# Kernel tuning notes

Measured on AMD Instinct MI355X. Metric: run time of the kernel, lower is better.

## Reference

```python
import jax, jax.numpy as jnp
import numpy as np

N, E = 20000, 200000
HID, NH, L = 128, 8, 7
DH = HID // NH
SCALE = float(np.sqrt(DH))
NNUM = 5
MLP_IN = HID + HID + 8 + 8 + 8 + NNUM  # 285
EPS = 1e-5


def _ln(x, g, b):
    mu = jnp.mean(x, -1, keepdims=True)
    var = jnp.mean((x - mu) ** 2, -1, keepdims=True)
    return (x - mu) * jax.lax.rsqrt(var + EPS) * g + b


def setup_inputs() -> dict:
    key = jax.random.key(0)
    ks = jax.random.split(key, 24)
    f = lambda k, s: (0.05 * jax.random.normal(k, s)).astype(jnp.float32)
    z = lambda s: jnp.zeros(s, jnp.float32)
    o = lambda s: jnp.ones(s, jnp.float32)
    inp = {
        'node_feats': f(ks[0], (N, 2)),
        'numericals': f(ks[1], (E, NNUM)),
        'W_emb': f(ks[2], (2, HID)), 'b_emb': z((HID,)),
        'WQ': f(ks[3], (L, HID, HID)), 'bQ': z((L, HID)),
        'WK': f(ks[4], (L, HID, HID)), 'bK': z((L, HID)),
        'WV': f(ks[5], (L, HID, HID)), 'bV': z((L, HID)),
        'WO': f(ks[6], (L, HID, HID)), 'bO': z((L, HID)),
        'ln1_g': o((L, HID)), 'ln1_b': z((L, HID)),
        'ln2_g': o((L, HID)), 'ln2_b': z((L, HID)),
        'W1': f(ks[7], (L, HID, HID)), 'b1': z((L, HID)),
        'W2': f(ks[8], (L, HID, HID)), 'b2': z((L, HID)),
        'curr_emb': f(ks[9], (15, 8)), 'pay_emb': f(ks[10], (7, 8)),
        'mlp_Wh': f(ks[11], (3, MLP_IN, MLP_IN)), 'mlp_bh': z((3, MLP_IN)),
        'mlp_Wo': f(ks[12], (MLP_IN, 2)), 'mlp_bo': z((2,)),
        'src': jax.random.randint(ks[13], (E,), 0, N, dtype=jnp.int32),
        'dst': jax.random.randint(ks[14], (E,), 0, N, dtype=jnp.int32),
        'payment_currency': jax.random.randint(ks[15], (E,), 0, 15, dtype=jnp.int32),
        'receiving_currency': jax.random.randint(ks[16], (E,), 0, 15, dtype=jnp.int32),
        'payment_format': jax.random.randint(ks[17], (E,), 0, 7, dtype=jnp.int32),
    }
    return inp


def reference(node_feats, numericals, W_emb, b_emb, WQ, bQ, WK, bK, WV, bV, WO, bO,
              ln1_g, ln1_b, ln2_g, ln2_b, W1, b1, W2, b2, curr_emb, pay_emb,
              mlp_Wh, mlp_bh, mlp_Wo, mlp_bo, src, dst,
              payment_currency, receiving_currency, payment_format):
    h = node_feats @ W_emb + b_emb  # [N, HID]
    for l in range(L):
        # --- graph multi-head attention (segment softmax over in-edges of dst) ---
        x = _ln(h, ln1_g[l], ln1_b[l])
        Q = (x @ WQ[l] + bQ[l]).reshape(N, NH, DH)
        K = (x @ WK[l] + bK[l]).reshape(N, NH, DH)
        V = (x @ WV[l] + bV[l]).reshape(N, NH, DH)
        scores = jnp.einsum('ehd,ehd->eh', Q[dst], K[src]) / SCALE  # [E, NH]
        m = jax.ops.segment_max(scores, dst, num_segments=N)        # [N, NH]
        ex = jnp.exp(scores - m[dst])
        den = jax.ops.segment_sum(ex, dst, num_segments=N)
        w = ex / den[dst]                                           # attn weights per edge
        attn = jax.ops.segment_sum(w[:, :, None] * V[src], dst, num_segments=N)
        h = h + attn.reshape(N, HID) @ WO[l] + bO[l]
        # --- FFN ---
        x = _ln(h, ln2_g[l], ln2_b[l])
        h = h + jax.nn.relu(x @ W1[l] + b1[l]) @ W2[l] + b2[l]
    # --- edge classifier ---
    ef = jnp.concatenate([curr_emb[payment_currency], curr_emb[receiving_currency],
                          pay_emb[payment_format], numericals], axis=1)  # [E, 29]
    y = jnp.concatenate([h[src], h[dst], ef], axis=1)  # [E, 285]
    for i in range(3):
        y = jax.nn.relu(y @ mlp_Wh[i] + mlp_bh[i])
    return y @ mlp_Wo + mlp_bo  # [E, 2]
```

## Files before the change

kernel.cpp:

```cpp
#include <hip/hip_runtime.h>

#define HID 128
#define NH 8
#define DH 16
#define NLAYERS 7
#define MLP_IN 285
#define MP 288
#define LDW 296
#define XS 136

typedef short short8 __attribute__((ext_vector_type(8)));
typedef float f32x4 __attribute__((ext_vector_type(4)));
typedef float f32x16 __attribute__((ext_vector_type(16)));
typedef unsigned short ushort8 __attribute__((ext_vector_type(8)));

__device__ inline unsigned short f2bf(float f) {
    union { float f; unsigned int u; } v; v.f = f;
    unsigned int r = v.u + 0x7FFF + ((v.u >> 16) & 1);
    return (unsigned short)(r >> 16);
}
__device__ inline float bf2f(unsigned short u) {
    union { unsigned int u; float f; } v; v.u = ((unsigned int)u) << 16;
    return v.f;
}

__global__ __launch_bounds__(256) void embed_kernel(
    const float* __restrict__ nf, const float* __restrict__ We,
    const float* __restrict__ be, float* __restrict__ h, int N)
{
    int idx = blockIdx.x * 256 + threadIdx.x;
    if (idx >= N * HID) return;
    int n = idx >> 7, j = idx & 127;
    h[idx] = fmaf(nf[n * 2], We[j], fmaf(nf[n * 2 + 1], We[HID + j], be[j]));
}

__global__ __launch_bounds__(256) void prep_nodew_kernel(
    const float* __restrict__ WQ, const float* __restrict__ WK,
    const float* __restrict__ WV, const float* __restrict__ WO,
    const float* __restrict__ W1, const float* __restrict__ W2,
    unsigned short* __restrict__ wnh, unsigned short* __restrict__ wnl)
{
    int idx = blockIdx.x * 256 + threadIdx.x;
    if (idx >= 42 * 32 * 64) return;
    int lane = idx & 63;
    int r = idx >> 6;
    int kt = r & 7; r >>= 3;
    int ct = r & 3; r >>= 2;
    int m = r;
    int l = m / 6, wi = m - l * 6;
    const float* Wb;
    switch (wi) {
        case 0: Wb = WQ; break; case 1: Wb = WK; break; case 2: Wb = WV; break;
        case 3: Wb = WO; break; case 4: Wb = W1; break; default: Wb = W2; break;
    }
    Wb += (size_t)l * HID * HID;
    int n = ct * 32 + (lane & 31);
    int kb = kt * 16 + (lane >> 5) * 8;
    ushort8 vh, vl;
#pragma unroll
    for (int j = 0; j < 8; ++j) {
        float w = Wb[(size_t)(kb + j) * HID + n];
        unsigned short hi = f2bf(w);
        vh[j] = hi;
        vl[j] = f2bf(w - bf2f(hi));
    }
    *(ushort8*)&wnh[(size_t)idx * 8] = vh;
    *(ushort8*)&wnl[(size_t)idx * 8] = vl;
}

#define LOADB(m, BH, BL) do { \
    size_t fb_ = (((size_t)(matbase + (m)) * 32 + (size_t)wave * 8) * 64 + lane) * 8; \
    const unsigned short* Bh_ = wnh + fb_; \
    const unsigned short* Bl_ = wnl + fb_; \
    _Pragma("unroll") \
    for (int kt = 0; kt < 8; ++kt) { \
        BH[kt] = *(const short8*)&Bh_[kt * 512]; \
        BL[kt] = *(const short8*)&Bl_[kt * 512]; \
    } \
} while (0)

#define COMPSTORE(BH, BL, BIAS, OUT, STRIDE, OFF) do { \
    f32x16 acc = {}; \
    _Pragma("unroll") \
    for (int kt = 0; kt < 8; ++kt) \
        acc = __builtin_amdgcn_mfma_f32_32x32x16_bf16(ah[kt], BH[kt], acc, 0, 0, 0); \
    _Pragma("unroll") \
    for (int kt = 0; kt < 8; ++kt) \
        acc = __builtin_amdgcn_mfma_f32_32x32x16_bf16(al[kt], BH[kt], acc, 0, 0, 0); \
    _Pragma("unroll") \
    for (int kt = 0; kt < 8; ++kt) \
        acc = __builtin_amdgcn_mfma_f32_32x32x16_bf16(ah[kt], BL[kt], acc, 0, 0, 0); \
    int col_ = wave * 32 + l31; \
    float bv_ = (BIAS)[col_]; \
    _Pragma("unroll") \
    for (int r = 0; r < 16; ++r) { \
        int rowm_ = (r & 3) + 8 * (r >> 2) + 4 * half; \
        int row_ = rowBase + rowm_; \
        if (row_ < M) (OUT)[(size_t)row_ * (STRIDE) + (OFF) + col_] = acc[r] + bv_; \
    } \
} while (0)

__global__ __launch_bounds__(256, 2) void ln_qkv_mfma(
    const float* __restrict__ h,
    const float* __restrict__ g, const float* __restrict__ bb,
    const unsigned short* __restrict__ wnh, const unsigned short* __restrict__ wnl,
    int matbase,
    const float* __restrict__ bQ, const float* __restrict__ bK, const float* __restrict__ bV,
    float* __restrict__ qo, float* __restrict__ kvo, int M)
{
    __shared__ unsigned short Xh[32][XS];
    __shared__ unsigned short Xl[32][XS];
    int tid = threadIdx.x;
    int lane = tid & 63, wave = tid >> 6;
    int rowBase = blockIdx.x * 32;

    for (int i = 0; i < 8; ++i) {
        int r = wave * 8 + i;
        int row = rowBase + r;
        float a0 = 0.f, a1 = 0.f;
        if (row < M) {
            a0 = h[(size_t)row * HID + lane];
            a1 = h[(size_t)row * HID + 64 + lane];
        }
        float s = a0 + a1;
#pragma unroll
        for (int off = 32; off > 0; off >>= 1) s += __shfl_down(s, off, 64);
        s = __shfl(s, 0, 64);
        float mu = s * (1.0f / 128.0f);
        float d0 = a0 - mu, d1 = a1 - mu;
        float v = d0 * d0 + d1 * d1;
#pragma unroll
        for (int off = 32; off > 0; off >>= 1) v += __shfl_down(v, off, 64);
        v = __shfl(v, 0, 64);
        float rr = rsqrtf(v * (1.0f / 128.0f) + 1e-5f);
        float x0 = d0 * rr * g[lane] + bb[lane];
        float x1 = d1 * rr * g[64 + lane] + bb[64 + lane];
        unsigned short h0 = f2bf(x0), h1 = f2bf(x1);
        Xh[r][lane] = h0;           Xh[r][64 + lane] = h1;
        Xl[r][lane] = f2bf(x0 - bf2f(h0));
        Xl[r][64 + lane] = f2bf(x1 - bf2f(h1));
    }
    __syncthreads();

    int l31 = lane & 31;
    int half = lane >> 5;

    short8 ah[8], al[8];
#pragma unroll
    for (int kt = 0; kt < 8; ++kt) {
        ah[kt] = *(const short8*)&Xh[l31][kt * 16 + half * 8];
        al[kt] = *(const short8*)&Xl[l31][kt * 16 + half * 8];
    }

    short8 bh0[8], bl0[8], bh1[8], bl1[8];
    LOADB(0, bh0, bl0);
    LOADB(1, bh1, bl1);
    COMPSTORE(bh0, bl0, bQ, qo, HID, 0);
    LOADB(2, bh0, bl0);
    COMPSTORE(bh1, bl1, bK, kvo, 256, 0);
    COMPSTORE(bh0, bl0, bV, kvo, 256, 128);
}

__global__ __launch_bounds__(256, 2) void post_qkv_mfma(
    const float* __restrict__ at, const float* __restrict__ hin,
    const unsigned short* __restrict__ wnh, const unsigned short* __restrict__ wnl,
    int matbase,
    const float* __restrict__ bO,
    const float* __restrict__ g2, const float* __restrict__ b2g,
    const float* __restrict__ b1, const float* __restrict__ b2,
    float* __restrict__ hout,
    int doQkv,
    const float* __restrict__ g1n, const float* __restrict__ b1n,
    const float* __restrict__ bQn, const float* __restrict__ bKn, const float* __restrict__ bVn,
    float* __restrict__ qout, float* __restrict__ kvout,
    unsigned short* __restrict__ hbout,
    int M)
{
    __shared__ unsigned short Ah[32][XS];
    __shared__ unsigned short Al[32][XS];
    __shared__ unsigned short Th[32][XS];
    __shared__ unsigned short Tl[32][XS];
    __shared__ float Hs[32][132];
    int tid = threadIdx.x;
    int lane = tid & 63, wave = tid >> 6;
    int rowBase = blockIdx.x * 32;
    int l31 = lane & 31;
    int half = lane >> 5;

    for (int i = tid; i < 32 * 32; i += 256) {
        int r = i >> 5, c4 = i & 31;
        int row = rowBase + r;
        float4 va = make_float4(0.f, 0.f, 0.f, 0.f), vh = va;
        if (row < M) {
            va = *(const float4*)&at[(size_t)row * HID + c4 * 4];
            vh = *(const float4*)&hin[(size_t)row * HID + c4 * 4];
        }
        const float* vp = (const float*)&va;
#pragma unroll
        for (int q = 0; q < 4; ++q) {
            unsigned short hi = f2bf(vp[q]);
            Ah[r][c4 * 4 + q] = hi;
            Al[r][c4 * 4 + q] = f2bf(vp[q] - bf2f(hi));
        }
        *(float4*)&Hs[r][c4 * 4] = vh;
    }
    __syncthreads();

    int colW = wave * 32 + l31;

    {
        short8 ah[8], al[8];
#pragma unroll
        for (int kt = 0; kt < 8; ++kt) {
            ah[kt] = *(const short8*)&Ah[l31][kt * 16 + half * 8];
            al[kt] = *(const short8*)&Al[l31][kt * 16 + half * 8];
        }
        short8 bh[8], bl[8];
        {
            size_t fb = (((size_t)(matbase + 3) * 32 + (size_t)wave * 8) * 64 + lane) * 8;
            const unsigned short* Bh = wnh + fb;
            const unsigned short* Bl = wnl + fb;
#pragma unroll
            for (int kt = 0; kt < 8; ++kt) {
                bh[kt] = *(const short8*)&Bh[kt * 512];
                bl[kt] = *(const short8*)&Bl[kt * 512];
            }
        }
        f32x16 acc = {};
#pragma unroll
        for (int kt = 0; kt < 8; ++kt)
            acc = __builtin_amdgcn_mfma_f32_32x32x16_bf16(ah[kt], bh[kt], acc, 0, 0, 0);
#pragma unroll
        for (int kt = 0; kt < 8; ++kt)
            acc = __builtin_amdgcn_mfma_f32_32x32x16_bf16(al[kt], bh[kt], acc, 0, 0, 0);
#pragma unroll
        for (int kt = 0; kt < 8; ++kt)
            acc = __builtin_amdgcn_mfma_f32_32x32x16_bf16(ah[kt], bl[kt], acc, 0, 0, 0);
        float bv = bO[colW];
#pragma unroll
        for (int r = 0; r < 16; ++r) {
            int rowm = (r & 3) + 8 * (r >> 2) + 4 * half;
            Hs[rowm][colW] += acc[r] + bv;
        }
    }
    __syncthreads();

    for (int i = 0; i < 8; ++i) {
        int r = wave * 8 + i;
        float a0 = Hs[r][lane];
        float a1 = Hs[r][64 + lane];
        float s = a0 + a1;
#pragma unroll
        for (int off = 32; off > 0; off >>= 1) s += __shfl_down(s, off, 64);
        s = __shfl(s, 0, 64);
        float mu = s * (1.0f / 128.0f);
        float d0 = a0 - mu, d1 = a1 - mu;
        float v = d0 * d0 + d1 * d1;
#pragma unroll
        for (int off = 32; off > 0; off >>= 1) v += __shfl_down(v, off, 64);
        v = __shfl(v, 0, 64);
        float rr = rsqrtf(v * (1.0f / 128.0f) + 1e-5f);
        float x0 = d0 * rr * g2[lane] + b2g[lane];
        float x1 = d1 * rr * g2[64 + lane] + b2g[64 + lane];
        unsigned short h0 = f2bf(x0), h1 = f2bf(x1);
        Ah[r][lane] = h0;           Ah[r][64 + lane] = h1;
        Al[r][lane] = f2bf(x0 - bf2f(h0));
        Al[r][64 + lane] = f2bf(x1 - bf2f(h1));
    }
    __syncthreads();

    {
        short8 ah[8], al[8];
#pragma unroll
        for (int kt = 0; kt < 8; ++kt) {
            ah[kt] = *(const short8*)&Ah[l31][kt * 16 + half * 8];
            al[kt] = *(const short8*)&Al[l31][kt * 16 + half * 8];
        }
        short8 bh[8], bl[8];
        {
            size_t fb = (((size_t)(matbase + 4) * 32 + (size_t)wave * 8) * 64 + lane) * 8;
            const unsigned short* Bh = wnh + fb;
            const unsigned short* Bl = wnl + fb;
#pragma unroll
            for (int kt = 0; kt < 8; ++kt) {
                bh[kt] = *(const short8*)&Bh[kt * 512];
                bl[kt] = *(const short8*)&Bl[kt * 512];
            }
        }
        f32x16 acc = {};
#pragma unroll
        for (int kt = 0; kt < 8; ++kt)
            acc = __builtin_amdgcn_mfma_f32_32x32x16_bf16(ah[kt], bh[kt], acc, 0, 0, 0);
#pragma unroll
        for (int kt = 0; kt < 8; ++kt)
            acc = __builtin_amdgcn_mfma_f32_32x32x16_bf16(al[kt], bh[kt], acc, 0, 0, 0);
#pragma unroll
        for (int kt = 0; kt < 8; ++kt)
            acc = __builtin_amdgcn_mfma_f32_32x32x16_bf16(ah[kt], bl[kt], acc, 0, 0, 0);
        float bv = b1[colW];
#pragma unroll
        for (int r = 0; r < 16; ++r) {
            int rowm = (r & 3) + 8 * (r >> 2) + 4 * half;
            float t = fmaxf(acc[r] + bv, 0.f);
            unsigned short hi = f2bf(t);
            Th[rowm][colW] = hi;
            Tl[rowm][colW] = f2bf(t - bf2f(hi));
        }
    }
    __syncthreads();

    {
        short8 ah[8], al[8];
#pragma unroll
        for (int kt = 0; kt < 8; ++kt) {
            ah[kt] = *(const short8*)&Th[l31][kt * 16 + half * 8];
            al[kt] = *(const short8*)&Tl[l31][kt * 16 + half * 8];
        }
        short8 bh[8], bl[8];
        {
            size_t fb = (((size_t)(matbase + 5) * 32 + (size_t)wave * 8) * 64 + lane) * 8;
            const unsigned short* Bh = wnh + fb;
            const unsigned short* Bl = wnl + fb;
#pragma unroll
            for (int kt = 0; kt < 8; ++kt) {
                bh[kt] = *(const short8*)&Bh[kt * 512];
                bl[kt] = *(const short8*)&Bl[kt * 512];
            }
        }
        f32x16 acc = {};
#pragma unroll
        for (int kt = 0; kt < 8; ++kt)
            acc = __builtin_amdgcn_mfma_f32_32x32x16_bf16(ah[kt], bh[kt], acc, 0, 0, 0);
#pragma unroll
        for (int kt = 0; kt < 8; ++kt)
            acc = __builtin_amdgcn_mfma_f32_32x32x16_bf16(al[kt], bh[kt], acc, 0, 0, 0);
#pragma unroll
        for (int kt = 0; kt < 8; ++kt)
            acc = __builtin_amdgcn_mfma_f32_32x32x16_bf16(ah[kt], bl[kt], acc, 0, 0, 0);
        float bv = b2[colW];
#pragma unroll
        for (int r = 0; r < 16; ++r) {
            int rowm = (r & 3) + 8 * (r >> 2) + 4 * half;
            int row = rowBase + rowm;
            float hn = Hs[rowm][colW] + acc[r] + bv;
            Hs[rowm][colW] = hn;
            if (row < M) {
                if (doQkv) hout[(size_t)row * HID + colW] = hn;
                else       hbout[(size_t)row * HID + colW] = f2bf(hn);
            }
        }
    }

    if (!doQkv) return;
    __syncthreads();

    for (int i = 0; i < 8; ++i) {
        int r = wave * 8 + i;
        float a0 = Hs[r][lane];
        float a1 = Hs[r][64 + lane];
        float s = a0 + a1;
#pragma unroll
        for (int off = 32; off > 0; off >>= 1) s += __shfl_down(s, off, 64);
        s = __shfl(s, 0, 64);
        float mu = s * (1.0f / 128.0f);
        float d0 = a0 - mu, d1 = a1 - mu;
        float v = d0 * d0 + d1 * d1;
#pragma unroll
        for (int off = 32; off > 0; off >>= 1) v += __shfl_down(v, off, 64);
        v = __shfl(v, 0, 64);
        float rr = rsqrtf(v * (1.0f / 128.0f) + 1e-5f);
        float x0 = d0 * rr * g1n[lane] + b1n[lane];
        float x1 = d1 * rr * g1n[64 + lane] + b1n[64 + lane];
        unsigned short h0 = f2bf(x0), h1 = f2bf(x1);
        Ah[r][lane] = h0;           Ah[r][64 + lane] = h1;
        Al[r][lane] = f2bf(x0 - bf2f(h0));
        Al[r][64 + lane] = f2bf(x1 - bf2f(h1));
    }
    __syncthreads();

    {
        short8 ah[8], al[8];
#pragma unroll
        for (int kt = 0; kt < 8; ++kt) {
            ah[kt] = *(const short8*)&Ah[l31][kt * 16 + half * 8];
            al[kt] = *(const short8*)&Al[l31][kt * 16 + half * 8];
        }
        short8 bh0[8], bl0[8], bh1[8], bl1[8];
        LOADB(6, bh0, bl0);
        LOADB(7, bh1, bl1);
        COMPSTORE(bh0, bl0, bQn, qout, HID, 0);
        LOADB(8, bh0, bl0);
        COMPSTORE(bh1, bl1, bKn, kvout, 256, 0);
        COMPSTORE(bh0, bl0, bVn, kvout, 256, 128);
    }
}

__global__ __launch_bounds__(256) void deg_kernel(
    const int* __restrict__ dst, int* __restrict__ deg, int E)
{
    int e = blockIdx.x * 256 + threadIdx.x;
    if (e < E) atomicAdd(&deg[dst[e]], 1);
}

__global__ __launch_bounds__(256) void scan_kernel(
    const int* __restrict__ deg, int* __restrict__ rowptr,
    int* __restrict__ cursor, int N)
{
    __shared__ int sums[256];
    int tid = threadIdx.x;
    int chunk = (N + 255) / 256;
    int lo = tid * chunk;
    int hi = lo + chunk; if (hi > N) hi = N;
    int s = 0;
    for (int i = lo; i < hi && i >= 0; ++i) s += deg[i];
    sums[tid] = s;
    __syncthreads();
    for (int off = 1; off < 256; off <<= 1) {
        int v = (tid >= off) ? sums[tid - off] : 0;
        __syncthreads();
        sums[tid] += v;
        __syncthreads();
    }
    int base = (tid == 0) ? 0 : sums[tid - 1];
    for (int i = lo; i < hi; ++i) {
        rowptr[i] = base; cursor[i] = base; base += deg[i];
    }
    if (tid == 255) rowptr[N] = sums[255];
}

__global__ __launch_bounds__(256) void scatter_kernel(
    const int* __restrict__ src, const int* __restrict__ dst,
    int* __restrict__ cursor, int* __restrict__ ssrc, int E)
{
    int e = blockIdx.x * 256 + threadIdx.x;
    if (e < E) {
        int p = atomicAdd(&cursor[dst[e]], 1);
        ssrc[p] = src[e];
    }
}

__global__ __launch_bounds__(256) void attn_fused_kernel(
    const float* __restrict__ q, const float* __restrict__ kv,
    const int* __restrict__ rowptr, const int* __restrict__ ssrc,
    float* __restrict__ at, int N)
{
    int node = blockIdx.x * 4 + (threadIdx.x >> 6);
    int lane = threadIdx.x & 63;
    if (node >= N) return;
    int beg = rowptr[node], end = rowptr[node + 1];
    float q0 = q[(size_t)node * HID + lane];
    float q1 = q[(size_t)node * HID + 64 + lane];
    float acc0 = 0.f, acc1 = 0.f, den0 = 0.f, den1 = 0.f;
    int i = beg;
    for (; i + 2 <= end; i += 2) {
        int s0 = ssrc[i], s1 = ssrc[i + 1];
        const float* kv0 = kv + (size_t)s0 * 256;
        const float* kv1 = kv + (size_t)s1 * 256;
        float k00 = kv0[lane],       k01 = kv0[64 + lane];
        float v00 = kv0[128 + lane], v01 = kv0[192 + lane];
        float k10 = kv1[lane],       k11 = kv1[64 + lane];
        float v10 = kv1[128 + lane], v11 = kv1[192 + lane];
        float p00 = q0 * k00, p01 = q1 * k01;
        float p10 = q0 * k10, p11 = q1 * k11;
#pragma unroll
        for (int off = 1; off < 16; off <<= 1) {
            p00 += __shfl_xor(p00, off, 64);
            p01 += __shfl_xor(p01, off, 64);
            p10 += __shfl_xor(p10, off, 64);
            p11 += __shfl_xor(p11, off, 64);
        }
        float w00 = __expf(p00 * 0.25f), w01 = __expf(p01 * 0.25f);
        float w10 = __expf(p10 * 0.25f), w11 = __expf(p11 * 0.25f);
        den0 += w00 + w10; den1 += w01 + w11;
        acc0 = fmaf(w10, v10, fmaf(w00, v00, acc0));
        acc1 = fmaf(w11, v11, fmaf(w01, v01, acc1));
    }
    if (i < end) {
        int s = ssrc[i];
        const float* kv0 = kv + (size_t)s * 256;
        float k0 = kv0[lane], k1 = kv0[64 + lane];
        float p0 = q0 * k0, p1 = q1 * k1;
#pragma unroll
        for (int off = 1; off < 16; off <<= 1) {
            p0 += __shfl_xor(p0, off, 64);
            p1 += __shfl_xor(p1, off, 64);
        }
        float w0 = __expf(p0 * 0.25f), w1 = __expf(p1 * 0.25f);
        den0 += w0; den1 += w1;
        acc0 = fmaf(w0, kv0[128 + lane], acc0);
        acc1 = fmaf(w1, kv0[192 + lane], acc1);
    }
    at[(size_t)node * HID + lane]      = (den0 > 0.f) ? acc0 / den0 : 0.f;
    at[(size_t)node * HID + 64 + lane] = (den1 > 0.f) ? acc1 / den1 : 0.f;
}

__global__ __launch_bounds__(256) void prep_wp_kernel(
    const float* __restrict__ Wh, unsigned short* __restrict__ wp)
{
    int idx = blockIdx.x * 256 + threadIdx.x;
    if (idx >= 3 * 9 * 18 * 64) return;
    int lane = idx & 63;
    int r = idx >> 6;
    int kt = r % 18; r /= 18;
    int ct = r % 9;
    int layer = r / 9;
    int n = ct * 32 + (lane & 31);
    int kbase = kt * 16 + (lane >> 5) * 8;
    ushort8 val;
#pragma unroll
    for (int j = 0; j < 8; ++j) {
        int k = kbase + j;
        float v = (n < MLP_IN && k < MLP_IN)
            ? Wh[(size_t)layer * MLP_IN * MLP_IN + (size_t)k * MLP_IN + n] : 0.f;
        val[j] = f2bf(v);
    }
    *(ushort8*)&wp[(size_t)idx * 8] = val;
}

__global__ __launch_bounds__(256, 3) void edge_mlp_mfma(
    const unsigned short* __restrict__ hb, const float* __restrict__ ce,
    const float* __restrict__ pe, const float* __restrict__ num,
    const int* __restrict__ src, const int* __restrict__ dst,
    const int* __restrict__ pc, const int* __restrict__ rc,
    const int* __restrict__ pf,
    const unsigned short* __restrict__ wp, const float* __restrict__ bh,
    const float* __restrict__ Wo, const float* __restrict__ bo,
    float* __restrict__ out, int E)
{
    __shared__ unsigned short y[64 * LDW];
    __shared__ float sc[2][32][33];
    int tid = threadIdx.x;
    int e0 = blockIdx.x * 64;
    int wave = tid >> 6;
    int lane = tid & 63;
    int l31 = lane & 31;
    int half = lane >> 5;

    for (int i = tid; i < 64 * 36; i += 256) {
        int t = i / 36;
        int c = i - t * 36;
        int e = e0 + t;
        if (e >= E) e = E - 1;
        ushort8 val;
        if (c < 16) {
            val = *(const ushort8*)&hb[(size_t)src[e] * HID + c * 8];
        } else if (c < 32) {
            val = *(const ushort8*)&hb[(size_t)dst[e] * HID + (c - 16) * 8];
        } else if (c == 32) {
            const float* p = &ce[pc[e] * 8];
#pragma unroll
            for (int j = 0; j < 8; ++j) val[j] = f2bf(p[j]);
        } else if (c == 33) {
            const float* p = &ce[rc[e] * 8];
#pragma unroll
            for (int j = 0; j < 8; ++j) val[j] = f2bf(p[j]);
        } else if (c == 34) {
            const float* p = &pe[pf[e] * 8];
#pragma unroll
            for (int j = 0; j < 8; ++j) val[j] = f2bf(p[j]);
        } else {
            const float* p = &num[(size_t)e * 5];
#pragma unroll
            for (int j = 0; j < 5; ++j) val[j] = f2bf(p[j]);
            val[5] = 0; val[6] = 0; val[7] = 0;
        }
        *(ushort8*)&y[t * LDW + c * 8] = val;
    }
    __syncthreads();

    int slab = wave & 1;
    int kh = wave >> 1;
    int rowA = slab * 32 + l31;

    for (int layer = 0; layer < 3; ++layer) {
        const float* __restrict__ bias = bh + layer * MLP_IN;

        short8 afr[9];
#pragma unroll
        for (int k = 0; k < 9; ++k)
            afr[k] = *(const short8*)&y[rowA * LDW + (kh * 9 + k) * 16 + half * 8];
        __syncthreads();

        for (int ct = 0; ct < 9; ++ct) {
            const unsigned short* __restrict__ Bp =
                wp + (size_t)layer * 82944 + (size_t)ct * 9216
                   + (size_t)(kh * 9) * 512 + (size_t)lane * 8;
            short8 bfr[9];
#pragma unroll
            for (int k = 0; k < 9; ++k)
                bfr[k] = *(const short8*)&Bp[k * 512];
            f32x16 acc = {};
#pragma unroll
            for (int k = 0; k < 9; ++k)
                acc = __builtin_amdgcn_mfma_f32_32x32x16_bf16(afr[k], bfr[k], acc, 0, 0, 0);

            if (kh == 1) {
#pragma unroll
                for (int r = 0; r < 16; ++r) {
                    int rowm = (r & 3) + 8 * (r >> 2) + 4 * half;
                    sc[slab][rowm][l31] = acc[r];
                }
            }
            __syncthreads();
            if (kh == 0) {
                int col = ct * 32 + l31;
                if (col < MLP_IN) {
                    float bv = bias[col];
#pragma unroll
                    for (int r = 0; r < 16; ++r) {
                        int rowm = (r & 3) + 8 * (r >> 2) + 4 * half;
                        float t = fmaxf(acc[r] + sc[slab][rowm][l31] + bv, 0.f);
                        y[(slab * 32 + rowm) * LDW + col] = f2bf(t);
                    }
                }
            }
            __syncthreads();
        }
    }

    {
        int t = tid >> 2;
        int oc = tid & 1;
        int kk = (tid >> 1) & 1;
        int e = e0 + t;
        const unsigned short* yr = &y[t * LDW];
        float p0 = 0.f, p1 = 0.f, p2 = 0.f, p3 = 0.f;
        int kc_lo = kk ? 18 : 0;
        int kc_hi = kk ? 35 : 18;
        for (int kc = kc_lo; kc < kc_hi; ++kc) {
            ushort8 yv = *(const ushort8*)&yr[kc * 8];
            int kb = kc * 8;
            p0 = fmaf(bf2f(yv[0]), Wo[(kb + 0) * 2 + oc], p0);
            p1 = fmaf(bf2f(yv[1]), Wo[(kb + 1) * 2 + oc], p1);
            p2 = fmaf(bf2f(yv[2]), Wo[(kb + 2) * 2 + oc], p2);
            p3 = fmaf(bf2f(yv[3]), Wo[(kb + 3) * 2 + oc], p3);
            p0 = fmaf(bf2f(yv[4]), Wo[(kb + 4) * 2 + oc], p0);
            p1 = fmaf(bf2f(yv[5]), Wo[(kb + 5) * 2 + oc], p1);
            p2 = fmaf(bf2f(yv[6]), Wo[(kb + 6) * 2 + oc], p2);
            p3 = fmaf(bf2f(yv[7]), Wo[(kb + 7) * 2 + oc], p3);
        }
        float acc = (p0 + p1) + (p2 + p3);
        if (kk) {
            for (int k = 280; k < MLP_IN; ++k)
                acc = fmaf(bf2f(yr[k]), Wo[k * 2 + oc], acc);
        }
        acc += __shfl_xor(acc, 2, 64);
        if (kk == 0 && e < E)
            out[(size_t)e * 2 + oc] = acc + bo[oc];
    }
}

extern "C" void kernel_launch(void* const* d_in, const int* in_sizes, int n_in,
                              void* d_out, int out_size, void* d_ws, size_t ws_size,
                              hipStream_t stream)
{
    const float* node_feats = (const float*)d_in[0];
    const float* numericals = (const float*)d_in[1];
    const float* W_emb = (const float*)d_in[2];
    const float* b_emb = (const float*)d_in[3];
    const float* WQ = (const float*)d_in[4];
    const float* bQ = (const float*)d_in[5];
    const float* WK = (const float*)d_in[6];
    const float* bK = (const float*)d_in[7];
    const float* WV = (const float*)d_in[8];
    const float* bV = (const float*)d_in[9];
    const float* WO = (const float*)d_in[10];
    const float* bO = (const float*)d_in[11];
    const float* ln1_g = (const float*)d_in[12];
    const float* ln1_b = (const float*)d_in[13];
    const float* ln2_g = (const float*)d_in[14];
    const float* ln2_b = (const float*)d_in[15];
    const float* W1 = (const float*)d_in[16];
    const float* b1 = (const float*)d_in[17];
    const float* W2 = (const float*)d_in[18];
    const float* b2 = (const float*)d_in[19];
    const float* curr_emb = (const float*)d_in[20];
    const float* pay_emb = (const float*)d_in[21];
    const float* mlp_Wh = (const float*)d_in[22];
    const float* mlp_bh = (const float*)d_in[23];
    const float* mlp_Wo = (const float*)d_in[24];
    const float* mlp_bo = (const float*)d_in[25];
    const int* src = (const int*)d_in[26];
    const int* dst = (const int*)d_in[27];
    const int* pc = (const int*)d_in[28];
    const int* rc = (const int*)d_in[29];
    const int* pf = (const int*)d_in[30];

    const int N = in_sizes[0] / 2;
    const int E = in_sizes[26];

    float* ws = (float*)d_ws;
    float* h    = ws;
    float* qb0  = h    + (size_t)N * HID;
    float* kvb0 = qb0  + (size_t)N * HID;
    float* qb1  = kvb0 + (size_t)N * HID * 2;
    float* kvb1 = qb1  + (size_t)N * HID;
    float* at   = kvb1 + (size_t)N * HID * 2;
    unsigned short* hb = (unsigned short*)(at + (size_t)N * HID);
    unsigned short* wpk = hb + (size_t)N * HID;
    unsigned short* wnh = wpk + (size_t)3 * 9 * 18 * 64 * 8;
    unsigned short* wnl = wnh + (size_t)42 * 32 * 64 * 8;
    int* rowptr = (int*)(wnl + (size_t)42 * 32 * 64 * 8);
    int* deg    = rowptr + (N + 1);
    int* cursor = deg + N;
    int* ssrc   = cursor + N;

    prep_wp_kernel<<<(3 * 9 * 18 * 64 + 255) / 256, 256, 0, stream>>>(mlp_Wh, wpk);
    prep_nodew_kernel<<<(42 * 32 * 64 + 255) / 256, 256, 0, stream>>>(
        WQ, WK, WV, WO, W1, W2, wnh, wnl);

    embed_kernel<<<(N * HID + 255) / 256, 256, 0, stream>>>(node_feats, W_emb, b_emb, h, N);

    hipMemsetAsync(deg, 0, (size_t)N * sizeof(int), stream);
    deg_kernel<<<(E + 255) / 256, 256, 0, stream>>>(dst, deg, E);
    scan_kernel<<<1, 256, 0, stream>>>(deg, rowptr, cursor, N);
    scatter_kernel<<<(E + 255) / 256, 256, 0, stream>>>(src, dst, cursor, ssrc, E);

    int nodeBlocks = (N + 31) / 32;

    ln_qkv_mfma<<<nodeBlocks, 256, 0, stream>>>(
        h, ln1_g, ln1_b, wnh, wnl, 0,
        bQ, bK, bV, qb0, kvb0, N);

    float* qbuf[2]  = { qb0, qb1 };
    float* kvbuf[2] = { kvb0, kvb1 };

    for (int l = 0; l < NLAYERS; ++l) {
        int cur = l & 1, nxt = cur ^ 1;
        int doQkv = (l < NLAYERS - 1) ? 1 : 0;
        int ln = (l + 1 < NLAYERS) ? (l + 1) : 0;

        attn_fused_kernel<<<(N + 3) / 4, 256, 0, stream>>>(
            qbuf[cur], kvbuf[cur], rowptr, ssrc, at, N);

        post_qkv_mfma<<<nodeBlocks, 256, 0, stream>>>(
            at, h, wnh, wnl, l * 6,
            bO + l * HID,
            ln2_g + l * HID, ln2_b + l * HID,
            b1 + l * HID, b2 + l * HID,
            h, doQkv,
            ln1_g + ln * HID, ln1_b + ln * HID,
            bQ + ln * HID, bK + ln * HID, bV + ln * HID,
            qbuf[nxt], kvbuf[nxt],
            hb, N);
    }

    edge_mlp_mfma<<<(E + 63) / 64, 256, 0, stream>>>(
        hb, curr_emb, pay_emb, numericals, src, dst, pc, rc, pf,
        wpk, mlp_bh, mlp_Wo, mlp_bo, (float*)d_out, E);
}
```

Before: 1.108 ms.

## Split edge MLP by output columns instead of K halves; add sched barriers

```diff
diff --git a/kernel.cpp b/kernel.cpp
--- a/kernel.cpp
+++ b/kernel.cpp
@@ -77,6 +77,7 @@
         BH[kt] = *(const short8*)&Bh_[kt * 512]; \
         BL[kt] = *(const short8*)&Bl_[kt * 512]; \
     } \
+    __builtin_amdgcn_sched_barrier(0); \
 } while (0)
 
 #define COMPSTORE(BH, BL, BIAS, OUT, STRIDE, OFF) do { \
@@ -225,6 +226,7 @@
                 bh[kt] = *(const short8*)&Bh[kt * 512];
                 bl[kt] = *(const short8*)&Bl[kt * 512];
             }
+            __builtin_amdgcn_sched_barrier(0);
         }
         f32x16 acc = {};
 #pragma unroll
@@ -286,6 +288,7 @@
                 bh[kt] = *(const short8*)&Bh[kt * 512];
                 bl[kt] = *(const short8*)&Bl[kt * 512];
             }
+            __builtin_amdgcn_sched_barrier(0);
         }
         f32x16 acc = {};
 #pragma unroll
@@ -326,6 +329,7 @@
                 bh[kt] = *(const short8*)&Bh[kt * 512];
                 bl[kt] = *(const short8*)&Bl[kt * 512];
             }
+            __builtin_amdgcn_sched_barrier(0);
         }
         f32x16 acc = {};
 #pragma unroll
@@ -517,7 +521,7 @@
     *(ushort8*)&wp[(size_t)idx * 8] = val;
 }
 
-__global__ __launch_bounds__(256, 3) void edge_mlp_mfma(
+__global__ __launch_bounds__(256, 2) void edge_mlp_mfma(
     const unsigned short* __restrict__ hb, const float* __restrict__ ce,
     const float* __restrict__ pe, const float* __restrict__ num,
     const int* __restrict__ src, const int* __restrict__ dst,
@@ -528,7 +532,6 @@
     float* __restrict__ out, int E)
 {
     __shared__ unsigned short y[64 * LDW];
-    __shared__ float sc[2][32][33];
     int tid = threadIdx.x;
     int e0 = blockIdx.x * 64;
     int wave = tid >> 6;
@@ -568,54 +571,44 @@
     }
     __syncthreads();
 
-    int slab = wave & 1;
-    int kh = wave >> 1;
+    int slab = wave >> 1;
     int rowA = slab * 32 + l31;
+    int ctlo = (wave & 1) ? 5 : 0;
+    int cthi = (wave & 1) ? 9 : 5;
 
     for (int layer = 0; layer < 3; ++layer) {
         const float* __restrict__ bias = bh + layer * MLP_IN;
 
-        short8 afr[9];
-#pragma unroll
-        for (int k = 0; k < 9; ++k)
-            afr[k] = *(const short8*)&y[rowA * LDW + (kh * 9 + k) * 16 + half * 8];
+        short8 afr[18];
+#pragma unroll
+        for (int kt = 0; kt < 18; ++kt)
+            afr[kt] = *(const short8*)&y[rowA * LDW + kt * 16 + half * 8];
         __syncthreads();
 
-        for (int ct = 0; ct < 9; ++ct) {
+        for (int ct = ctlo; ct < cthi; ++ct) {
             const unsigned short* __restrict__ Bp =
-                wp + (size_t)layer * 82944 + (size_t)ct * 9216
-                   + (size_t)(kh * 9) * 512 + (size_t)lane * 8;
-            short8 bfr[9];
-#pragma unroll
-            for (int k = 0; k < 9; ++k)
-                bfr[k] = *(const short8*)&Bp[k * 512];
+                wp + (size_t)layer * 82944 + (size_t)ct * 9216 + (size_t)lane * 8;
+            short8 bfr[18];
+#pragma unroll
+            for (int kt = 0; kt < 18; ++kt)
+                bfr[kt] = *(const short8*)&Bp[kt * 512];
+            __builtin_amdgcn_sched_barrier(0);
             f32x16 acc = {};
 #pragma unroll
-            for (int k = 0; k < 9; ++k)
-                acc = __builtin_amdgcn_mfma_f32_32x32x16_bf16(afr[k], bfr[k], acc, 0, 0, 0);
-
-            if (kh == 1) {
+            for (int kt = 0; kt < 18; ++kt)
+                acc = __builtin_amdgcn_mfma_f32_32x32x16_bf16(afr[kt], bfr[kt], acc, 0, 0, 0);
+            int col = ct * 32 + l31;
+            if (col < MLP_IN) {
+                float bv = bias[col];
 #pragma unroll
                 for (int r = 0; r < 16; ++r) {
                     int rowm = (r & 3) + 8 * (r >> 2) + 4 * half;
-                    sc[slab][rowm][l31] = acc[r];
+                    float t = fmaxf(acc[r] + bv, 0.f);
+                    y[(slab * 32 + rowm) * LDW + col] = f2bf(t);
                 }
             }
-            __syncthreads();
-            if (kh == 0) {
-                int col = ct * 32 + l31;
-                if (col < MLP_IN) {
-                    float bv = bias[col];
-#pragma unroll
-                    for (int r = 0; r < 16; ++r) {
-                        int rowm = (r & 3) + 8 * (r >> 2) + 4 * half;
-                        float t = fmaxf(acc[r] + sc[slab][rowm][l31] + bv, 0.f);
-                        y[(slab * 32 + rowm) * LDW + col] = f2bf(t);
-                    }
-                }
-            }
-            __syncthreads();
-        }
+        }
+        __syncthreads();
     }
 
     {
```

New measurement: 1.077 ms. 1.03x faster.
